# Performance work log

Hardware: AMD Instinct MI355X
Metric: run time of the kernel (lower is better)

Reference implementation:

```python
import jax, jax.numpy as jnp
import numpy as np

EPS_BN = 1e-5
K_INTERP = 8
K_NEIGH = 16


def _bn(x, g, b):
    # BatchNorm1d in training mode: batch stats over rows (biased var), eps=1e-5
    m = x.mean(axis=0)
    v = x.var(axis=0)
    return (x - m) * jax.lax.rsqrt(v + EPS_BN) * g + b


def _dist(a, b):
    # a:(B,N,3), b:(B,M,3) -> Euclidean distance (B,N,M), computed via the
    # quadratic expansion (clamped at 0) instead of materializing (B,N,M,3)
    d2 = (jnp.sum(a * a, -1)[:, :, None] + jnp.sum(b * b, -1)[:, None, :]
          - 2.0 * jnp.einsum('bnc,bmc->bnm', a, b))
    return jnp.sqrt(jnp.maximum(d2, 0.0))


def _gather(feats, idx):
    # feats:(B,M,C), idx:(B,N,K) int -> (B,N,K,C)
    return jax.vmap(lambda f, i: f[i])(feats, idx)


def setup_inputs() -> dict:
    key = jax.random.key(0)
    B, N1, N2, DS, DD, DOUT = 4, 4096, 1024, 128, 64, 256
    ks = jax.random.split(key, 20)
    s = 0.02
    inp = {
        'p1': jax.random.uniform(ks[0], (B * N1, 3), jnp.float32),
        'x1': jax.random.normal(ks[1], (B * N1, DD), jnp.float32),
        'o1': (jnp.arange(B, dtype=jnp.int32) + 1) * N1,
        'p2': jax.random.uniform(ks[2], (B * N2, 3), jnp.float32),
        'x2': jax.random.normal(ks[3], (B * N2, DS), jnp.float32),
        'o2': (jnp.arange(B, dtype=jnp.int32) + 1) * N2,
        'batch_size': B,
        # dense_mlp: Linear(DD,DS) + BN
        'W_dense': jax.random.normal(ks[4], (DD, DS), jnp.float32) * s,
        'b_dense': jnp.zeros((DS,), jnp.float32),
        'g_dense': jnp.ones((DS,), jnp.float32),
        'bt_dense': jnp.zeros((DS,), jnp.float32),
        # CrossAttentionPointTransformerLayer (dim=DS, hidden_mult=1)
        'Wq': jax.random.normal(ks[5], (DS, DS), jnp.float32) * s,
        'Wk': jax.random.normal(ks[6], (DS, DS), jnp.float32) * s,
        'Wv': jax.random.normal(ks[7], (DS, DS), jnp.float32) * s,
        'W1': jax.random.normal(ks[8], (DS, DS), jnp.float32) * s,
        'b1': jnp.zeros((DS,), jnp.float32),
        'g1': jnp.ones((DS,), jnp.float32),
        'bt1': jnp.zeros((DS,), jnp.float32),
        'W2': jax.random.normal(ks[9], (DS, DS), jnp.float32) * s,
        'b2': jnp.zeros((DS,), jnp.float32),
        # output mlp: Linear(DS+DD, DOUT) + BN
        'W_out': jax.random.normal(ks[10], (DS + DD, DOUT), jnp.float32) * s,
        'b_out': jnp.zeros((DOUT,), jnp.float32),
        'g_out': jnp.ones((DOUT,), jnp.float32),
        'bt_out': jnp.zeros((DOUT,), jnp.float32),
    }
    return inp


def reference(p1, x1, o1, p2, x2, o2, batch_size,
              W_dense, b_dense, g_dense, bt_dense,
              Wq, Wk, Wv, W1, b1, g1, bt1, W2, b2,
              W_out, b_out, g_out, bt_out):
    B = int(batch_size)
    N1 = p1.shape[0] // B
    N2 = p2.shape[0] // B
    DS = x2.shape[-1]

    # dense_mlp
    x1_dense = jax.nn.relu(_bn(x1 @ W_dense + b_dense, g_dense, bt_dense))  # (B*N1, DS)

    # pointops.interpolation(p2, p1, x2, o2, o1, k=8): inverse-distance kNN interp
    p1b = p1.reshape(B, N1, 3)
    p2b = p2.reshape(B, N2, 3)
    x2b = x2.reshape(B, N2, DS)
    d12 = _dist(p1b, p2b)                       # (B,N1,N2)
    negd, idx = jax.lax.top_k(-d12, K_INTERP)   # k nearest in p2
    dknn = -negd
    recip = 1.0 / (dknn + 1e-8)
    w = recip / recip.sum(-1, keepdims=True)    # (B,N1,8)
    x2_interp = jnp.einsum('bnk,bnkc->bnc', w, _gather(x2b, idx))  # (B,N1,DS)

    # CrossAttentionPointTransformerLayer(x_e=x1_dense, x_r=x_d=x2_interp, pos=p1)
    x_e = x1_dense.reshape(B, N1, DS)
    q = x_e @ Wq
    k = x2_interp @ Wk
    v = x2_interp @ Wv
    rel_dist = _dist(p1b, p1b)                  # (B,N1,N1)
    _, nidx = jax.lax.top_k(-rel_dist, K_NEIGH) # 16 nearest neighbors
    kg = _gather(k, nidx)                        # (B,N1,16,DS)
    vg = _gather(v, nidx)
    xeg = _gather(x_e, nidx)
    qk_rel = q[:, :, None, :] - kg
    v2 = vg + xeg
    h = (qk_rel + xeg).reshape(-1, DS)           # (B*N1*16, DS)
    h = jax.nn.relu(_bn(h @ W1 + b1, g1, bt1))
    sim = (h @ W2 + b2).reshape(B, N1, K_NEIGH, DS)
    attn = jax.nn.softmax(sim, axis=-2)          # over neighbors
    agg = jnp.einsum('bnkc,bnkc->bnc', attn, v2).reshape(B * N1, DS)

    # output mlp
    x = jax.nn.relu(_bn(jnp.concatenate([agg, x1], axis=-1) @ W_out + b_out,
                        g_out, bt_out))
    return (p1, x, o1)
```

## Files before the change

kernel.cpp:

```cpp
#include <hip/hip_runtime.h>
#include <math.h>

#define BB 4
#define NN1 4096
#define NN2 1024
#define DS 128
#define DD 64
#define DOUT 256
#define M1 16384
#define MH 262144
#define KCAT 192
#define KI 8
#define KN 16

#define OUT_P1 49152
#define OUT_X  49152
#define OUT_O1 4243456


static const size_t OFF_HPRE = 0;
static const size_t OFF_WTS  = 16777216;
static const size_t OFF_TMP  = 33554432;
static const size_t OFF_XD   = OFF_TMP  + 2097152;
static const size_t OFF_XI   = OFF_XD   + 2097152;
static const size_t OFF_Q    = OFF_XI   + 2097152;
static const size_t OFF_K    = OFF_Q    + 2097152;
static const size_t OFF_V    = OFF_K    + 2097152;
static const size_t OFF_OUTP = OFF_V    + 2097152;
static const size_t OFF_NIDX = OFF_OUTP + 4194304;
static const size_t OFF_STAT = OFF_NIDX + 262144;
static const size_t OFF_P1Q  = OFF_STAT + 4096;
static const size_t OFF_P2Q  = OFF_P1Q  + 65536;
static const size_t OFF_P1S  = OFF_P2Q  + 16384;
static const size_t OFF_P2S  = OFF_P1S  + 65536;

#define WDH 0
#define WDL 8192
#define WQH 16384
#define WQL 32768
#define WKH 49152
#define WKL 65536
#define WVH 81920
#define WVL 98304
#define W1H 114688
#define W1L 131072
#define W2H 147456
#define W2L 163840
#define WOH 180224
#define WOL 229376

typedef __attribute__((ext_vector_type(8))) short short8;
typedef __attribute__((ext_vector_type(4))) float floatx4;
typedef __attribute__((ext_vector_type(2))) float float2v;

__device__ inline unsigned short f2bf(float f) {
    union { float f; unsigned int u; } x; x.f = f;
    unsigned int r = x.u + 0x7fffu + ((x.u >> 16) & 1u);
    return (unsigned short)(r >> 16);
}
__device__ inline float bf2f(unsigned short h) {
    union { unsigned int u; float f; } x; x.u = ((unsigned int)h) << 16;
    return x.f;
}
__device__ inline unsigned long long shfl_xor_u64(unsigned long long v, int m) {
    unsigned lo = (unsigned)v, hi = (unsigned)(v >> 32);
    lo = (unsigned)__shfl_xor((int)lo, m);
    hi = (unsigned)__shfl_xor((int)hi, m);
    return ((unsigned long long)hi << 32) | lo;
}
__device__ inline unsigned cvt_pk_bf16(float lo, float hi) {
    unsigned r;
    asm volatile("v_cvt_pk_bf16_f32 %0, %1, %2" : "=v"(r) : "v"(lo), "v"(hi));
    return r;
}

#define PRO_STAT  (OUT_P1 + BB)
#define PRO_PACK  (PRO_STAT + 3072)
#define PRO_TOTAL (PRO_PACK + M1 + BB*NN2)
#define NPRO 285
struct SwzParams {
    const float* W[7];
    unsigned short* hi[7];
    unsigned short* lo[7];
    int N[7];
    int fid0[8];
};
__global__ __launch_bounds__(256) void k_prolog(
    const float* __restrict__ p1, const int* __restrict__ o1,
    const float* __restrict__ p2, float* __restrict__ out,
    float* __restrict__ stat, float4* __restrict__ p1q,
    float4* __restrict__ p2q, float* __restrict__ p1s,
    float* __restrict__ p2s, SwzParams p)
{
    if (blockIdx.x < NPRO) {
        int i = blockIdx.x * 256 + threadIdx.x;
        if (i < OUT_P1) out[i] = p1[i];
        else if (i < PRO_STAT) out[OUT_O1 + (i - OUT_P1)] = (float)o1[i - OUT_P1];
        else if (i < PRO_PACK) stat[i - PRO_STAT] = 0.f;
        else if (i < PRO_TOTAL) {
            int j = i - PRO_PACK;
            const float* src; float4* dst; float* ps; int jj;
            if (j < M1) { src = p1; dst = p1q; ps = p1s; jj = j; }
            else        { src = p2; dst = p2q; ps = p2s; jj = j - M1; }
            float x = src[jj*3+0] * 16384.f;
            float y = src[jj*3+1] * 16384.f;
            float z = src[jj*3+2] * 16384.f;
            float n = fmaf(z, z, fmaf(y, y, x*x));
            dst[jj] = make_float4(x, y, z, n);
            int pb8 = (jj >> 1)*8 + (jj & 1);
            ps[pb8]   = x + x; ps[pb8+2] = y + y;
            ps[pb8+4] = z + z; ps[pb8+6] = n;
        }
        return;
    }
    int fid = (blockIdx.x - NPRO)*4 + (threadIdx.x >> 6);
    int lane = threadIdx.x & 63;
    if (fid >= 272) return;
    int seg = 0;
    #pragma unroll
    for (int i = 1; i < 7; i++) if (fid >= p.fid0[i]) seg = i;
    int f = fid - p.fid0[seg];
    const float* W = p.W[seg];
    int N = p.N[seg];
    int ncj = N >> 4;
    int slab = f / ncj, cj = f - slab*ncj;
    int n  = cj*16 + (lane & 15);
    int k0 = slab*32 + (lane >> 4)*8;
    unsigned int oh[8], ol[8];
    #pragma unroll
    for (int j = 0; j < 8; j++) {
        float v = W[(size_t)(k0 + j) * N + n];
        unsigned short h = f2bf(v);
        oh[j] = h;
        ol[j] = f2bf(v - bf2f(h));
    }
    uint4 ph, pl;
    ph.x = oh[0] | (oh[1] << 16); ph.y = oh[2] | (oh[3] << 16);
    ph.z = oh[4] | (oh[5] << 16); ph.w = oh[6] | (oh[7] << 16);
    pl.x = ol[0] | (ol[1] << 16); pl.y = ol[2] | (ol[3] << 16);
    pl.z = ol[4] | (ol[5] << 16); pl.w = ol[6] | (ol[7] << 16);
    ((uint4*)p.hi[seg])[f*64 + lane] = ph;
    ((uint4*)p.lo[seg])[f*64 + lane] = pl;
}

template<int N, int K, int MODE, int STATS, int BNA>
__global__ __launch_bounds__(256) void k_gemm_mf(
    const float* __restrict__ Amat, const unsigned short* __restrict__ Whi,
    const unsigned short* __restrict__ Wlo, const float* __restrict__ bias,
    float* __restrict__ C, const float* __restrict__ aux,
    float* __restrict__ sums, float* __restrict__ sumsq,
    const float* __restrict__ bsums, const float* __restrict__ bsumsq,
    const float* __restrict__ bg, const float* __restrict__ bbt)
{
    __shared__ float sstat[STATS ? 2*N : 1];
    __shared__ float sbn[BNA ? 2*DS : 1];
    const int t = threadIdx.x, w = t >> 6, lane = t & 63;
    const int quad = lane >> 4, c = lane & 15;
    const int row = blockIdx.x*64 + w*16 + c;
    const int sA = (MODE == 2) ? DS : K;
    constexpr int nslab = K >> 5;
    constexpr int ncj = N >> 4;
    const int seg = (MODE == 3) ? blockIdx.y : 0;
    const float* Abase = (MODE == 3 && seg > 0) ? aux : Amat;
    const unsigned short* WhiS = Whi + (size_t)seg*32768;
    const unsigned short* WloS = Wlo + (size_t)seg*32768;
    float* CS = C + (size_t)seg*2097152;
    unsigned short* CS16 = (unsigned short*)C + (size_t)seg*4194304;
    if (STATS) {
        for (int i = t; i < 2*N; i += 256) sstat[i] = 0.f;
    }
    if (BNA) {
        if (t < DS) {
            const float invM = 1.f / (float)M1;
            float m   = bsums[t] * invM;
            float var = bsumsq[t] * invM - m*m;
            float sc  = bg[t] * rsqrtf(var + 1e-5f);
            sbn[t] = sc;
            sbn[DS + t] = bbt[t] - m * sc;
        }
    }
    if (STATS || BNA) __syncthreads();

    floatx4 acc[ncj];
    #pragma unroll
    for (int cj = 0; cj < ncj; cj++) acc[cj] = (floatx4){0.f,0.f,0.f,0.f};

    #pragma unroll
    for (int slab = 0; slab < nslab; slab++) {
        const int kk = slab*32 + quad*8;
        const float* src;
        if (MODE == 2 && kk >= DS) src = aux + (size_t)row*DD + (kk - DS);
        else                       src = Abase + (size_t)row*sA + kk;
        floatx4 va = *(const floatx4*)src;
        floatx4 vb = *(const floatx4*)(src + 4);
        if (BNA && MODE == 3 && seg == 0) {
            #pragma unroll
            for (int j = 0; j < 4; j++) {
                va[j] = fmaxf(fmaf(va[j], sbn[kk+j],   sbn[DS+kk+j]),   0.f);
                vb[j] = fmaxf(fmaf(vb[j], sbn[kk+4+j], sbn[DS+kk+4+j]), 0.f);
            }
        }
        short8 ahi, alo;
        #pragma unroll
        for (int j = 0; j < 4; j++) {
            unsigned short h = f2bf(va[j]);
            ahi[j] = (short)h; alo[j] = (short)f2bf(va[j] - bf2f(h));
        }
        #pragma unroll
        for (int j = 0; j < 4; j++) {
            unsigned short h = f2bf(vb[j]);
            ahi[4+j] = (short)h; alo[4+j] = (short)f2bf(vb[j] - bf2f(h));
        }
        const short8* bh = (const short8*)WhiS + (size_t)slab*ncj*64;
        const short8* bl = (const short8*)WloS + (size_t)slab*ncj*64;
        #pragma unroll
        for (int cj = 0; cj < ncj; cj++) {
            short8 bhv = bh[cj*64 + lane];
            short8 blv = bl[cj*64 + lane];
            acc[cj] = __builtin_amdgcn_mfma_f32_16x16x32_bf16(alo, bhv, acc[cj], 0, 0, 0);
            acc[cj] = __builtin_amdgcn_mfma_f32_16x16x32_bf16(ahi, blv, acc[cj], 0, 0, 0);
            acc[cj] = __builtin_amdgcn_mfma_f32_16x16x32_bf16(ahi, bhv, acc[cj], 0, 0, 0);
        }
    }
    const int rbase = blockIdx.x*64 + w*16 + quad*4;
    #pragma unroll
    for (int cj = 0; cj < ncj; cj++) {
        const float bb = bias ? bias[cj*16 + c] : 0.f;
        float s = 0.f, ss = 0.f;
        #pragma unroll
        for (int p = 0; p < 4; p++) {
            float v = acc[cj][p] + bb;
            if (MODE == 3) {
                if (seg > 0) {
                    float xv = Amat[(size_t)(rbase + p)*DS + cj*16 + c];
                    if (BNA) xv = fmaxf(fmaf(xv, sbn[cj*16+c], sbn[DS+cj*16+c]), 0.f);
                    if (seg == 1) v = xv - v;
                    else          v += xv;
                }
                CS16[(size_t)(rbase + p)*N + cj*16 + c] = f2bf(v);
            } else {
                CS[(size_t)(rbase + p)*N + cj*16 + c] = v;
            }
            if (STATS) { s += v; ss += v*v; }
        }
        if (STATS) {
            s  += __shfl_xor(s, 16);  s  += __shfl_xor(s, 32);
            ss += __shfl_xor(ss, 16); ss += __shfl_xor(ss, 32);
            if (quad == 0) {
                atomicAdd(&sstat[cj*16 + c], s);
                atomicAdd(&sstat[N + cj*16 + c], ss);
            }
        }
    }
    if (STATS) {
        __syncthreads();
        for (int i = t; i < N; i += 256) {
            atomicAdd(&sums[i],  sstat[i]);
            atomicAdd(&sumsq[i], sstat[N + i]);
        }
    }
}

__global__ __launch_bounds__(256) void k_gemm_qe(
    const unsigned short* __restrict__ q16, const unsigned short* __restrict__ e16,
    const unsigned short* __restrict__ W1hi, const float* __restrict__ b1,
    float* __restrict__ qw, float* __restrict__ ew)
{
    const int t = threadIdx.x, w = t >> 6, lane = t & 63;
    const int quad = lane >> 4, c = lane & 15;
    const int y = blockIdx.y;
    const unsigned short* A = y ? e16 : q16;
    float* C = y ? ew : qw;
    const int row = blockIdx.x*64 + w*16 + c;

    floatx4 acc[8];
    #pragma unroll
    for (int cj = 0; cj < 8; cj++) acc[cj] = (floatx4){0.f,0.f,0.f,0.f};

    #pragma unroll
    for (int slab = 0; slab < 4; slab++) {
        uint4 av = *(const uint4*)(A + (size_t)row*DS + slab*32 + quad*8);
        short8 af;
        ((uint4*)&af)[0] = av;
        const short8* bh = (const short8*)W1hi + (size_t)slab*8*64;
        #pragma unroll
        for (int cj = 0; cj < 8; cj++) {
            short8 bhv = bh[cj*64 + lane];
            acc[cj] = __builtin_amdgcn_mfma_f32_16x16x32_bf16(af, bhv, acc[cj], 0, 0, 0);
        }
    }
    const int rbase = blockIdx.x*64 + w*16 + quad*4;
    #pragma unroll
    for (int cj = 0; cj < 8; cj++) {
        const float bb = y ? b1[cj*16 + c] : 0.f;
        #pragma unroll
        for (int p = 0; p < 4; p++)
            C[(size_t)(rbase + p)*DS + cj*16 + c] = acc[cj][p] + bb;
    }
}

__global__ __launch_bounds__(256) void k_hstat(
    const float* __restrict__ qw, const float* __restrict__ ew,
    const int* __restrict__ nidx,
    float* __restrict__ sums, float* __restrict__ sumsq)
{
    __shared__ float sstat[256];
    const int t = threadIdx.x, w = t >> 6, lane = t & 63;
    sstat[t] = 0.f;
    __syncthreads();
    const int col = lane*2;
    float Sx = 0.f, Sy = 0.f, SSx = 0.f, SSy = 0.f;
    #pragma unroll
    for (int g2 = 0; g2 < 4; g2++) {
        const int gp = blockIdx.x*16 + w*4 + g2;
        float2 a = *(const float2*)(qw + (size_t)gp*DS + col);
        float B1x = 0.f, B1y = 0.f, B2x = 0.f, B2y = 0.f;
        const int* np = nidx + gp*16;
        #pragma unroll
        for (int cc = 0; cc < 16; cc++) {
            int m = np[cc];
            float2 b = *(const float2*)(ew + (size_t)m*DS + col);
            B1x += b.x; B1y += b.y;
            B2x = fmaf(b.x, b.x, B2x); B2y = fmaf(b.y, b.y, B2y);
        }
        Sx += fmaf(16.f, a.x, B1x);
        Sy += fmaf(16.f, a.y, B1y);
        SSx += fmaf(16.f*a.x, a.x, fmaf(2.f*a.x, B1x, B2x));
        SSy += fmaf(16.f*a.y, a.y, fmaf(2.f*a.y, B1y, B2y));
    }
    atomicAdd(&sstat[col],       Sx); atomicAdd(&sstat[col+1],       Sy);
    atomicAdd(&sstat[128 + col], SSx); atomicAdd(&sstat[128 + col+1], SSy);
    __syncthreads();
    if (t < 128) atomicAdd(&sums[t], sstat[t]);
    else         atomicAdd(&sumsq[t - 128], sstat[t]);
}

__global__ __launch_bounds__(256) void k_attn3(
    const float* __restrict__ qw, const float* __restrict__ ew,
    const float* __restrict__ sums_h, const float* __restrict__ sumsq_h,
    const float* __restrict__ g1, const float* __restrict__ bt1,
    const unsigned short* __restrict__ W2sw,
    const unsigned short* __restrict__ v, const int* __restrict__ nidx,
    float* __restrict__ agg)
{
    __shared__ unsigned short WF[16384];
    __shared__ float s_sc[DS], s_sh[DS];
    const int t = threadIdx.x;
    #pragma unroll
    for (int i = 0; i < 8; i++)
        ((uint4*)WF)[t + 256*i] = ((const uint4*)W2sw)[t + 256*i];
    if (t < DS) {
        const float invM = 1.f / (float)MH;
        float m   = sums_h[t] * invM;
        float var = sumsq_h[t] * invM - m*m;
        float sc  = g1[t] * rsqrtf(var + 1e-5f);
        s_sc[t] = sc;
        s_sh[t] = bt1[t] - m * sc;
    }
    __syncthreads();

    const int w = t >> 6, lane = t & 63;
    const int gp = blockIdx.x * 4 + w;
    const int quad = lane >> 4, c = lane & 15;
    const int mrow = nidx[gp*16 + c];

    floatx4 acc[8];
    #pragma unroll
    for (int cj = 0; cj < 8; cj++) acc[cj] = (floatx4){0.f, 0.f, 0.f, 0.f};

    for (int ks = 0; ks < 4; ks++) {
        const int ko = ks*32 + quad*8;
        const float* qp = qw + (size_t)gp*DS + ko;
        const float* ep = ew + (size_t)mrow*DS + ko;
        floatx4 qa = *(const floatx4*)qp;
        floatx4 qb = *(const floatx4*)(qp + 4);
        floatx4 ea = *(const floatx4*)ep;
        floatx4 eb = *(const floatx4*)(ep + 4);
        floatx4 sc0 = *(const floatx4*)&s_sc[ko];
        floatx4 sc1 = *(const floatx4*)&s_sc[ko + 4];
        floatx4 sh0 = *(const floatx4*)&s_sh[ko];
        floatx4 sh1 = *(const floatx4*)&s_sh[ko + 4];
        float f[8];
        #pragma unroll
        for (int j = 0; j < 4; j++) {
            f[j]   = fmaxf(fmaf(qa[j] + ea[j], sc0[j], sh0[j]), 0.f);
            f[4+j] = fmaxf(fmaf(qb[j] + eb[j], sc1[j], sh1[j]), 0.f);
        }
        short8 af;
        #pragma unroll
        for (int j = 0; j < 4; j++)
            ((unsigned*)&af)[j] = cvt_pk_bf16(f[2*j], f[2*j+1]);
        #pragma unroll
        for (int cj = 0; cj < 8; cj++) {
            short8 bfv = ((const short8*)WF)[(ks*8 + cj)*64 + lane];
            acc[cj] = __builtin_amdgcn_mfma_f32_16x16x32_bf16(af, bfv, acc[cj], 0, 0, 0);
        }
    }

    int nid[4];
    #pragma unroll
    for (int p = 0; p < 4; p++) nid[p] = nidx[gp*16 + quad*4 + p];

    #pragma unroll
    for (int cj = 0; cj < 8; cj++) {
        float m4 = fmaxf(fmaxf(acc[cj][0], acc[cj][1]), fmaxf(acc[cj][2], acc[cj][3]));
        m4 = fmaxf(m4, __shfl_xor(m4, 16));
        m4 = fmaxf(m4, __shfl_xor(m4, 32));
        float e[4]; float s4 = 0.f;
        #pragma unroll
        for (int p = 0; p < 4; p++) { e[p] = __expf(acc[cj][p] - m4); s4 += e[p]; }
        s4 += __shfl_xor(s4, 16); s4 += __shfl_xor(s4, 32);
        const float inv = 1.f / s4;
        const int col = cj*16 + c;
        float a = 0.f;
        #pragma unroll
        for (int p = 0; p < 4; p++)
            a = fmaf(e[p]*inv, bf2f(v[(size_t)nid[p]*DS + col]), a);
        a += __shfl_xor(a, 16); a += __shfl_xor(a, 32);
        if (quad == 0) agg[(size_t)gp*DS + col] = a;
    }
}

__global__ __launch_bounds__(256) void k_bnrelu(
    const float4* __restrict__ X, const float* __restrict__ sums,
    const float* __restrict__ sumsq, const float* __restrict__ g,
    const float* __restrict__ bt, float invM,
    float4* __restrict__ Y, size_t total4, int N)
{
    size_t i = (size_t)blockIdx.x * 256 + threadIdx.x;
    if (i < total4) {
        int c = (int)((i*4) & (size_t)(N - 1));
        float4 sm = *(const float4*)(sums + c);
        float4 sq = *(const float4*)(sumsq + c);
        float4 gg = *(const float4*)(g + c);
        float4 bb = *(const float4*)(bt + c);
        float4 x = X[i], y;
        float m0 = sm.x*invM, m1 = sm.y*invM, m2 = sm.z*invM, m3 = sm.w*invM;
        float s0 = gg.x*rsqrtf(sq.x*invM - m0*m0 + 1e-5f);
        float s1 = gg.y*rsqrtf(sq.y*invM - m1*m1 + 1e-5f);
        float s2 = gg.z*rsqrtf(sq.z*invM - m2*m2 + 1e-5f);
        float s3 = gg.w*rsqrtf(sq.w*invM - m3*m3 + 1e-5f);
        y.x = fmaxf(fmaf(x.x, s0, bb.x - m0*s0), 0.f);
        y.y = fmaxf(fmaf(x.y, s1, bb.y - m1*s1), 0.f);
        y.z = fmaxf(fmaf(x.z, s2, bb.z - m2*s2), 0.f);
        y.w = fmaxf(fmaf(x.w, s3, bb.w - m3*s3), 0.f);
        Y[i] = y;
    }
}

template<int NCAND, int KSEL, int EPI, int CAP>
__device__ __forceinline__ void sel_body(
    int gp0,
    const float4* __restrict__ qpts4, const float4* __restrict__ cpts4,
    const float* __restrict__ cpairs,
    int* __restrict__ nidx, const float* __restrict__ x2, float* __restrict__ xi,
    unsigned* hist0, unsigned* hist1,
    unsigned* skey, unsigned* sidx,
    float* swtE, unsigned* sidxE,
    unsigned* wpart, int* sstate)
{
    const int b = gp0 >> 12;
    const int t = threadIdx.x, wv = t >> 6, lane = t & 63;
    constexpr int ITER  = NCAND / 256;
    constexpr int PITER = NCAND / 512;

    const float4 qv0 = qpts4[gp0];
    const float4 qv1 = qpts4[gp0 + 1];
    const float4* pb = cpts4 + (size_t)b*NCAND;
    const float*  pbs = cpairs + (size_t)b*NCAND*4;

    unsigned kreg[2][ITER];
    if (t < 16)      ((uint4*)hist0)[t]      = (uint4){0u,0u,0u,0u};
    else if (t < 32) ((uint4*)hist1)[t - 16] = (uint4){0u,0u,0u,0u};
    __syncthreads();

    {
        const float2v nqx0 = {-qv0.x, -qv0.x}, nqy0 = {-qv0.y, -qv0.y};
        const float2v nqz0 = {-qv0.z, -qv0.z}, qw0 = {qv0.w, qv0.w};
        const float2v nqx1 = {-qv1.x, -qv1.x}, nqy1 = {-qv1.y, -qv1.y};
        const float2v nqz1 = {-qv1.z, -qv1.z}, qw1 = {qv1.w, qv1.w};
        #pragma unroll
        for (int pi = 0; pi < PITER; pi++) {
            const int ip = t + 256*pi;
            float4 A  = ((const float4*)pbs)[2*ip];
            float4 Bv = ((const float4*)pbs)[2*ip + 1];
            float2v xp = {A.x, A.y},  yp = {A.z, A.w};
            float2v zp = {Bv.x, Bv.y}, wp = {Bv.z, Bv.w};
            float2v d0 = wp + qw0;
            d0 = __builtin_elementwise_fma(xp, nqx0, d0);
            d0 = __builtin_elementwise_fma(yp, nqy0, d0);
            d0 = __builtin_elementwise_fma(zp, nqz0, d0);
            float2v d1 = wp + qw1;
            d1 = __builtin_elementwise_fma(xp, nqx1, d1);
            d1 = __builtin_elementwise_fma(yp, nqy1, d1);
            d1 = __builtin_elementwise_fma(zp, nqz1, d1);
            unsigned ka = (unsigned)d0[0], kb = (unsigned)d0[1];
            unsigned kc = (unsigned)d1[0], kd = (unsigned)d1[1];
            kreg[0][2*pi] = ka; kreg[0][2*pi+1] = kb;
            kreg[1][2*pi] = kc; kreg[1][2*pi+1] = kd;
            if ((ka >> 20) < CAP) atomicAdd(&hist0[ka >> 20], 1u);
            if ((kb >> 20) < CAP) atomicAdd(&hist0[kb >> 20], 1u);
            if ((kc >> 20) < CAP) atomicAdd(&hist1[kc >> 20], 1u);
            if ((kd >> 20) < CAP) atomicAdd(&hist1[kd >> 20], 1u);
        }
    }
    __syncthreads();

    if (wv < 2) {
        unsigned* H = wv ? hist1 : hist0;
        unsigned h = (lane < CAP) ? H[lane] : 0u;
        unsigned incl = h;
        #pragma unroll
        for (int off = 1; off < 64; off <<= 1) {
            unsigned o = (unsigned)__shfl_up((int)incl, off);
            if (lane >= off) incl += o;
        }
        unsigned excl = incl - h;
        const int base = wv*8;
        if ((int)excl < KSEL && KSEL <= (int)(excl + h)) {
            sstate[base+0] = lane; sstate[base+1] = (int)excl; sstate[base+2] = (int)h;
            sstate[base+3] = ((int)(excl + h) <= 64) ? 1 : 0;
            sstate[base+4] = 0;
        }
        unsigned tot = (unsigned)__shfl((int)incl, 63);
        if (lane == 0 && (int)tot < KSEL) sstate[base+3] = -1;
    }
    __syncthreads();

    if (sstate[3] == -1 || sstate[11] == -1) {
        for (int qi = 0; qi < 2; qi++) {
            if (sstate[qi*8+3] != -1) continue;
            ((uint4*)hist0)[t] = (uint4){0u,0u,0u,0u};
            __syncthreads();
            #pragma unroll
            for (int it = 0; it < ITER; it++)
                atomicAdd(&hist0[kreg[qi][it] >> 20], 1u);
            __syncthreads();
            uint4 h4 = ((const uint4*)hist0)[t];
            unsigned hv[4] = {h4.x, h4.y, h4.z, h4.w};
            unsigned tsum = hv[0]+hv[1]+hv[2]+hv[3];
            unsigned incl = tsum;
            #pragma unroll
            for (int off = 1; off < 64; off <<= 1) {
                unsigned o = (unsigned)__shfl_up((int)incl, off);
                if (lane >= off) incl += o;
            }
            if (lane == 63) wpart[wv] = incl;
            __syncthreads();
            unsigned wbase = 0;
            for (int i2 = 0; i2 < wv; i2++) wbase += wpart[i2];
            unsigned excl = wbase + incl - tsum;
            if ((int)excl < KSEL && KSEL <= (int)(excl + tsum)) {
                unsigned cum = excl;
                #pragma unroll
                for (int i2 = 0; i2 < 4; i2++) {
                    unsigned h = hv[i2];
                    if ((int)cum < KSEL && KSEL <= (int)(cum + h)) {
                        sstate[qi*8+0] = t*4 + i2; sstate[qi*8+1] = (int)cum;
                        sstate[qi*8+2] = (int)h;
                        sstate[qi*8+3] = ((int)cum + (int)h <= 64) ? 1 : 0;
                        sstate[qi*8+4] = 0;
                        break;
                    }
                    cum += h;
                }
            }
            __syncthreads();
        }
    }

    if (sstate[3] == 1 && sstate[11] == 1) {
        const unsigned P0 = (unsigned)sstate[0];
        const unsigned P1 = (unsigned)sstate[8];
        #pragma unroll
        for (int pi = 0; pi < PITER; pi++) {
            const int ip = t + 256*pi;
            #pragma unroll
            for (int c2 = 0; c2 < 2; c2++) {
                const int j = 2*ip + c2;
                const unsigned k0 = kreg[0][2*pi+c2], k1 = kreg[1][2*pi+c2];
                if ((k0 >> 20) <= P0) {
                    int pos = (int)atomicAdd((unsigned*)&sstate[4], 1u);
                    skey[pos] = k0; sidx[pos] = (unsigned)j;
                }
                if ((k1 >> 20) <= P1) {
                    int pos = (int)atomicAdd((unsigned*)&sstate[12], 1u);
                    skey[64 + pos] = k1; sidx[64 + pos] = (unsigned)j;
                }
            }
        }
    } else {
        #pragma unroll
        for (int qi = 0; qi < 2; qi++) {
            const float4 qv = qi ? qv1 : qv0;
            unsigned P = (unsigned)sstate[qi*8+0];
            int S = sstate[qi*8+1], cntB = sstate[qi*8+2], mode = sstate[qi*8+3];
            int gsh = 20;
            if (mode == 0) {
                for (int round = 1; round < 4; round++) {
                    const int nb  = (round == 3) ? 16 : 256;
                    const int wb  = (round == 3) ? 4 : 8;
                    const int sh  = (round == 1) ? 12 : (round == 2 ? 4 : 0);
                    const int psh = sh + wb;
                    if (t < nb) hist0[t] = 0u;
                    __syncthreads();
                    #pragma unroll
                    for (int it = 0; it < ITER; it++) {
                        unsigned key = kreg[qi][it];
                        if ((key >> psh) == P)
                            atomicAdd(&hist0[(key >> sh) & (nb - 1)], 1u);
                    }
                    __syncthreads();
                    unsigned hv = (t < nb) ? hist0[t] : 0u;
                    unsigned tsum = hv;
                    unsigned incl = tsum;
                    #pragma unroll
                    for (int off = 1; off < 64; off <<= 1) {
                        unsigned o = (unsigned)__shfl_up((int)incl, off);
                        if (lane >= off) incl += o;
                    }
                    if (lane == 63) wpart[wv] = incl;
                    __syncthreads();
                    unsigned wbase = 0;
                    for (int i2 = 0; i2 < wv; i2++) wbase += wpart[i2];
                    unsigned exclT = wbase + incl - tsum;
                    const int need = KSEL - S;
                    if ((int)exclT < need && need <= (int)(exclT + tsum)) {
                        int Snew = S + (int)exclT;
                        int tot  = Snew + (int)tsum;
                        sstate[qi*8+0] = (int)((P << wb) | (unsigned)t);
                        sstate[qi*8+1] = Snew; sstate[qi*8+2] = (int)tsum;
                        sstate[qi*8+3] = (tot <= 64) ? 1 : ((round == 3) ? 2 : 0);
                        sstate[qi*8+4] = 0;
                    }
                    __syncthreads();
                    P = (unsigned)sstate[qi*8+0]; S = sstate[qi*8+1];
                    cntB = sstate[qi*8+2]; mode = sstate[qi*8+3];
                    gsh = sh;
                    if (mode) break;
                }
            }
            if (mode == 1) {
                #pragma unroll
                for (int pi = 0; pi < PITER; pi++) {
                    const int ip = t + 256*pi;
                    #pragma unroll
                    for (int c2 = 0; c2 < 2; c2++) {
                        const int j = 2*ip + c2;
                        unsigned key = kreg[qi][2*pi+c2];
                        if ((key >> gsh) <= P) {
                            int pos = (int)atomicAdd((unsigned*)&sstate[qi*8+4], 1u);
                            skey[qi*64 + pos] = key; sidx[qi*64 + pos] = (unsigned)j;
                        }
                    }
                }
            } else if (mode != 1) {
                if (t < 64) {
                    const unsigned long long lmask = (1ull << lane) - 1ull;
                    int cnt = 0;
                    for (int pass = 0; pass < 2; pass++) {
                        for (int it = 0; it < NCAND/64; it++) {
                            int j = lane + 64*it;
                            float4 cv = pb[j];
                            float dot = fmaf(qv.z, cv.z, fmaf(qv.y, cv.y, qv.x*cv.x));
                            float d2 = fmaxf(fmaf(-2.f, dot, qv.w + cv.w), 0.f);
                            unsigned key = (unsigned)d2;
                            bool f = pass ? (key == P) : (key < P);
                            unsigned long long bal = __ballot(f);
                            if (f) {
                                int pos = cnt + __popcll(bal & lmask);
                                if (pos < 64) { skey[qi*64 + pos] = key; sidx[qi*64 + pos] = (unsigned)j; }
                            }
                            cnt += __popcll(bal);
                        }
                    }
                    if (lane == 0) { sstate[qi*8+1] = min(cnt, 64); sstate[qi*8+2] = 0; }
                }
            }
            __syncthreads();
        }
    }
    __syncthreads();

    if (wv < 2) {
        const int q = wv;
        const int total = sstate[q*8+1] + sstate[q*8+2];
        unsigned long long v = ~0ull;
        if (lane < total)
            v = (((unsigned long long)skey[q*64 + lane]) << 32) | sidx[q*64 + lane];
        #pragma unroll
        for (int k = 2; k <= 64; k <<= 1) {
            #pragma unroll
            for (int jj = k >> 1; jj > 0; jj >>= 1) {
                unsigned long long p = shfl_xor_u64(v, jj);
                bool up = ((lane & k) == 0);
                bool takeMin = (((lane & jj) == 0) == up);
                bool pl = p < v;
                v = (takeMin == pl) ? p : v;
            }
        }
        if (EPI == 0) {
            if (lane < KSEL)
                nidx[(gp0 + q)*KSEL + lane] = b*NCAND + (int)(v & 0xffffffffull);
        } else {
            const float4 qq = q ? qv1 : qv0;
            float wgt = 0.f;
            unsigned si = (unsigned)(v & 0xffffffffull);
            if (lane < KSEL) {
                float4 cv = pb[si];
                float dot = fmaf(qq.z, cv.z, fmaf(qq.y, cv.y, qq.x*cv.x));
                float d2 = fmaxf(fmaf(-2.f, dot, qq.w + cv.w), 0.f);
                wgt = 1.f / (sqrtf(d2) + 1.6384e-4f);
            }
            float ws = wgt;
            ws += __shfl_xor(ws, 1); ws += __shfl_xor(ws, 2); ws += __shfl_xor(ws, 4);
            if (lane < KSEL) {
                swtE[q*KSEL + lane]  = wgt / ws;
                sidxE[q*KSEL + lane] = si;
            }
        }
    }

    if (EPI == 1) {
        __syncthreads();
        const int qi2 = t >> 7, tt = t & 127;
        const float* x2b = x2 + (size_t)b*NCAND*DS;
        float a = 0.f;
        #pragma unroll
        for (int r = 0; r < KSEL; r++)
            a = fmaf(swtE[qi2*KSEL + r], x2b[(size_t)sidxE[qi2*KSEL + r]*DS + tt], a);
        xi[(size_t)(gp0 + qi2)*DS + tt] = a;
    }
}

__global__ __launch_bounds__(256) void k_sel2(
    const float4* __restrict__ p1q, const float4* __restrict__ p2q,
    const float* __restrict__ p1s, const float* __restrict__ p2s,
    int* __restrict__ nidx, const float* __restrict__ x2, float* __restrict__ xi)
{
    __shared__ __align__(16) unsigned hist0[1024], hist1[1024];
    __shared__ __align__(16) unsigned skey[128], sidx[128];
    __shared__ float    swtE[2*KI];
    __shared__ unsigned sidxE[2*KI];
    __shared__ unsigned wpart[8];
    __shared__ int      sstate[20];
    const int bid = blockIdx.x;
    if (bid < M1/2) {
        sel_body<NN1, KN, 0, 32>(bid*2, p1q, p1q, p1s, nidx, nullptr, nullptr,
                                 hist0, hist1, skey, sidx, swtE, sidxE, wpart, sstate);
    } else {
        sel_body<NN2, KI, 1, 64>((bid - M1/2)*2, p1q, p2q, p2s, nullptr, x2, xi,
                                 hist0, hist1, skey, sidx, swtE, sidxE, wpart, sstate);
    }
}

extern "C" void kernel_launch(void* const* d_in, const int* in_sizes, int n_in,
                              void* d_out, int out_size, void* d_ws, size_t ws_size,
                              hipStream_t stream)
{
    const float* p1 = (const float*)d_in[0];
    const float* x1 = (const float*)d_in[1];
    const int*   o1 = (const int*)d_in[2];
    const float* p2 = (const float*)d_in[3];
    const float* x2 = (const float*)d_in[4];
    const float* W_dense = (const float*)d_in[7];
    const float* b_dense = (const float*)d_in[8];
    const float* g_dense = (const float*)d_in[9];
    const float* bt_dense= (const float*)d_in[10];
    const float* Wq = (const float*)d_in[11];
    const float* Wk = (const float*)d_in[12];
    const float* Wv = (const float*)d_in[13];
    const float* W1 = (const float*)d_in[14];
    const float* b1 = (const float*)d_in[15];
    const float* g1 = (const float*)d_in[16];
    const float* bt1= (const float*)d_in[17];
    const float* W2 = (const float*)d_in[18];
    const float* W_out = (const float*)d_in[20];
    const float* b_out = (const float*)d_in[21];
    const float* g_out = (const float*)d_in[22];
    const float* bt_out= (const float*)d_in[23];

    float* ws   = (float*)d_ws;
    unsigned short* wts  = (unsigned short*)(ws + OFF_WTS);
    float* tmp  = ws + OFF_TMP;
    float* qw1f = ws + OFF_XD;
    float* ew1f = ws + OFF_OUTP;
    float* xi   = ws + OFF_XI;
    float* qm   = ws + OFF_Q;
    float* outp = ws + OFF_OUTP;
    int*   nidx = (int*)(ws + OFF_NIDX);
    float* stat = ws + OFF_STAT;
    float4* p1q = (float4*)(ws + OFF_P1Q);
    float4* p2q = (float4*)(ws + OFF_P2Q);
    float* p1s = ws + OFF_P1S;
    float* p2s = ws + OFF_P2S;
    unsigned short* q16 = (unsigned short*)(ws + OFF_Q);
    unsigned short* e16 = (unsigned short*)(ws + OFF_K);
    unsigned short* v16 = (unsigned short*)(ws + OFF_V);
    float* sums_d = stat,      *sumsq_d = stat+256;
    float* sums_h = stat+1024, *sumsq_h = stat+1280;
    float* sums_o = stat+2048, *sumsq_o = stat+2304;
    float* out = (float*)d_out;

    SwzParams sp;
    sp.W[0]=W_dense; sp.W[1]=Wq; sp.W[2]=Wk; sp.W[3]=Wv; sp.W[4]=W1; sp.W[5]=W2; sp.W[6]=W_out;
    sp.hi[0]=wts+WDH; sp.hi[1]=wts+WQH; sp.hi[2]=wts+WKH; sp.hi[3]=wts+WVH;
    sp.hi[4]=wts+W1H; sp.hi[5]=wts+W2H; sp.hi[6]=wts+WOH;
    sp.lo[0]=wts+WDL; sp.lo[1]=wts+WQL; sp.lo[2]=wts+WKL; sp.lo[3]=wts+WVL;
    sp.lo[4]=wts+W1L; sp.lo[5]=wts+W2L; sp.lo[6]=wts+WOL;
    sp.N[0]=128; sp.N[1]=128; sp.N[2]=128; sp.N[3]=128; sp.N[4]=128; sp.N[5]=128; sp.N[6]=256;
    sp.fid0[0]=0; sp.fid0[1]=16; sp.fid0[2]=48; sp.fid0[3]=80; sp.fid0[4]=112;
    sp.fid0[5]=144; sp.fid0[6]=176; sp.fid0[7]=272;
    k_prolog<<<NPRO + 68, 256, 0, stream>>>(p1, o1, p2, out, stat, p1q, p2q, p1s, p2s, sp);

    k_sel2<<<M1, 256, 0, stream>>>(p1q, p2q, p1s, p2s, nidx, x2, xi);

    k_gemm_mf<128,64,0,1,0><<<M1/64, 256, 0, stream>>>(x1, wts+WDH, wts+WDL, b_dense, tmp,
        nullptr, sums_d, sumsq_d, nullptr, nullptr, nullptr, nullptr);

    k_gemm_mf<128,128,3,0,1><<<dim3(M1/64,3), 256, 0, stream>>>(tmp, wts+WQH, wts+WQL,
        nullptr, qm, xi, nullptr, nullptr, sums_d, sumsq_d, g_dense, bt_dense);

    k_gemm_qe<<<dim3(M1/64, 2), 256, 0, stream>>>(q16, e16, wts+W1H, b1, qw1f, ew1f);
    k_hstat<<<M1/16, 256, 0, stream>>>(qw1f, ew1f, nidx, sums_h, sumsq_h);

    k_attn3<<<M1/4, 256, 0, stream>>>(qw1f, ew1f, sums_h, sumsq_h, g1, bt1,
        wts+W2H, v16, nidx, tmp);

    k_gemm_mf<256,192,2,1,0><<<M1/64, 256, 0, stream>>>(tmp, wts+WOH, wts+WOL, b_out, outp,
        x1, sums_o, sumsq_o, nullptr, nullptr, nullptr, nullptr);
    k_bnrelu<<<(M1*DOUT/4)/256, 256, 0, stream>>>((const float4*)outp, sums_o, sumsq_o,
        g_out, bt_out, 1.f/(float)M1, (float4*)(out + OUT_X), (size_t)M1*DOUT/4, DOUT);
}
```

Measured before the change: 322.0 us.

## Fold W1 into Wq/Wk products and store attention projections as bf16

Precomputes Wq·W1 and -Wk·W1 in the prolog so the Q-side and E-side W1 projections come directly out of the projection GEMMs. The separate k_gemm_qe pass and its fp32 intermediate buffers go away. The E-side becomes one K=256 GEMM over concatenated [x_e, x_interp] inputs, with BN+ReLU applied only to the x_e half. hstat and attn3 now read bf16 projections instead of fp32, which halves gather traffic at the cost of rounding error.

```diff
diff --git a/kernel.cpp b/kernel.cpp
--- a/kernel.cpp
+++ b/kernel.cpp
@@ -18,7 +18,6 @@
 #define OUT_O1 4243456
 
 
-static const size_t OFF_HPRE = 0;
 static const size_t OFF_WTS  = 16777216;
 static const size_t OFF_TMP  = 33554432;
 static const size_t OFF_XD   = OFF_TMP  + 2097152;
@@ -36,18 +35,16 @@
 
 #define WDH 0
 #define WDL 8192
-#define WQH 16384
-#define WQL 32768
-#define WKH 49152
-#define WKL 65536
+#define WQW1H 16384
+#define WQW1L 32768
 #define WVH 81920
 #define WVL 98304
-#define W1H 114688
-#define W1L 131072
-#define W2H 147456
-#define W2L 163840
-#define WOH 180224
-#define WOL 229376
+#define WEH 114688
+#define WEL 147456
+#define W2H 180224
+#define W2L 196608
+#define WOH 212992
+#define WOL 262144
 
 typedef __attribute__((ext_vector_type(8))) short short8;
 typedef __attribute__((ext_vector_type(4))) float floatx4;
@@ -79,11 +76,14 @@
 #define PRO_TOTAL (PRO_PACK + M1 + BB*NN2)
 #define NPRO 285
 struct SwzParams {
-    const float* W[7];
-    unsigned short* hi[7];
-    unsigned short* lo[7];
-    int N[7];
-    int fid0[8];
+    const float* W[5];
+    unsigned short* hi[5];
+    unsigned short* lo[5];
+    const float* Wq; const float* Wk; const float* W1r;
+    unsigned short* phi[2];
+    unsigned short* plo[2];
+    int N[5];
+    int fid0[5];
 };
 __global__ __launch_bounds__(256) void k_prolog(
     const float* __restrict__ p1, const int* __restrict__ o1,
@@ -116,31 +116,57 @@
     int fid = (blockIdx.x - NPRO)*4 + (threadIdx.x >> 6);
     int lane = threadIdx.x & 63;
     if (fid >= 272) return;
-    int seg = 0;
-    #pragma unroll
-    for (int i = 1; i < 7; i++) if (fid >= p.fid0[i]) seg = i;
-    int f = fid - p.fid0[seg];
-    const float* W = p.W[seg];
-    int N = p.N[seg];
-    int ncj = N >> 4;
-    int slab = f / ncj, cj = f - slab*ncj;
-    int n  = cj*16 + (lane & 15);
-    int k0 = slab*32 + (lane >> 4)*8;
+    float vsrc[8];
+    unsigned short* hiD; unsigned short* loD; int fstore;
+    if (fid < 208) {
+        int seg = 0;
+        #pragma unroll
+        for (int i = 1; i < 5; i++) if (fid >= p.fid0[i]) seg = i;
+        int f = fid - p.fid0[seg];
+        const float* W = p.W[seg];
+        int N = p.N[seg];
+        int ncj = N >> 4;
+        int slab = f / ncj, cj = f - slab*ncj;
+        int n  = cj*16 + (lane & 15);
+        int k0 = slab*32 + (lane >> 4)*8;
+        #pragma unroll
+        for (int j = 0; j < 8; j++) vsrc[j] = W[(size_t)(k0 + j) * N + n];
+        hiD = p.hi[seg]; loD = p.lo[seg]; fstore = f;
+    } else {
+        int pf = fid - 208;
+        int which = pf >> 5;
+        int f = pf & 31;
+        const float* Wa = which ? p.Wk : p.Wq;
+        int slab = f >> 3, cj = f & 7;
+        int n  = cj*16 + (lane & 15);
+        int k0 = slab*32 + (lane >> 4)*8;
+        float acc[8];
+        #pragma unroll
+        for (int j = 0; j < 8; j++) acc[j] = 0.f;
+        for (int m = 0; m < 128; m++) {
+            float wc = p.W1r[m*128 + n];
+            #pragma unroll
+            for (int j = 0; j < 8; j++)
+                acc[j] = fmaf(Wa[(size_t)(k0 + j)*128 + m], wc, acc[j]);
+        }
+        #pragma unroll
+        for (int j = 0; j < 8; j++) vsrc[j] = which ? -acc[j] : acc[j];
+        hiD = p.phi[which]; loD = p.plo[which]; fstore = f;
+    }
     unsigned int oh[8], ol[8];
     #pragma unroll
     for (int j = 0; j < 8; j++) {
-        float v = W[(size_t)(k0 + j) * N + n];
-        unsigned short h = f2bf(v);
+        unsigned short h = f2bf(vsrc[j]);
         oh[j] = h;
-        ol[j] = f2bf(v - bf2f(h));
+        ol[j] = f2bf(vsrc[j] - bf2f(h));
     }
     uint4 ph, pl;
     ph.x = oh[0] | (oh[1] << 16); ph.y = oh[2] | (oh[3] << 16);
     ph.z = oh[4] | (oh[5] << 16); ph.w = oh[6] | (oh[7] << 16);
     pl.x = ol[0] | (ol[1] << 16); pl.y = ol[2] | (ol[3] << 16);
     pl.z = ol[4] | (ol[5] << 16); pl.w = ol[6] | (ol[7] << 16);
-    ((uint4*)p.hi[seg])[f*64 + lane] = ph;
-    ((uint4*)p.lo[seg])[f*64 + lane] = pl;
+    ((uint4*)hiD)[fstore*64 + lane] = ph;
+    ((uint4*)loD)[fstore*64 + lane] = pl;
 }
 
 template<int N, int K, int MODE, int STATS, int BNA>
@@ -157,11 +183,11 @@
     const int t = threadIdx.x, w = t >> 6, lane = t & 63;
     const int quad = lane >> 4, c = lane & 15;
     const int row = blockIdx.x*64 + w*16 + c;
-    const int sA = (MODE == 2) ? DS : K;
+    const int sA = (MODE == 2 || MODE == 5) ? DS : K;
     constexpr int nslab = K >> 5;
     constexpr int ncj = N >> 4;
-    const int seg = (MODE == 3) ? blockIdx.y : 0;
-    const float* Abase = (MODE == 3 && seg > 0) ? aux : Amat;
+    const int seg = (MODE == 4) ? (int)blockIdx.y * 2 : 0;
+    const float* Abase = (MODE == 4 && seg > 0) ? aux : Amat;
     const unsigned short* WhiS = Whi + (size_t)seg*32768;
     const unsigned short* WloS = Wlo + (size_t)seg*32768;
     float* CS = C + (size_t)seg*2097152;
@@ -189,11 +215,12 @@
     for (int slab = 0; slab < nslab; slab++) {
         const int kk = slab*32 + quad*8;
         const float* src;
-        if (MODE == 2 && kk >= DS) src = aux + (size_t)row*DD + (kk - DS);
-        else                       src = Abase + (size_t)row*sA + kk;
+        if (MODE == 2 && kk >= DS)      src = aux + (size_t)row*DD + (kk - DS);
+        else if (MODE == 5 && kk >= DS) src = aux + (size_t)row*DS + (kk - DS);
+        else                            src = Abase + (size_t)row*sA + kk;
         floatx4 va = *(const floatx4*)src;
         floatx4 vb = *(const floatx4*)(src + 4);
-        if (BNA && MODE == 3 && seg == 0) {
+        if (BNA && ((MODE == 4 && seg == 0) || (MODE == 5 && kk < DS))) {
             #pragma unroll
             for (int j = 0; j < 4; j++) {
                 va[j] = fmaxf(fmaf(va[j], sbn[kk+j],   sbn[DS+kk+j]),   0.f);
@@ -230,12 +257,11 @@
         #pragma unroll
         for (int p = 0; p < 4; p++) {
             float v = acc[cj][p] + bb;
-            if (MODE == 3) {
-                if (seg > 0) {
+            if (MODE >= 4) {
+                if (MODE == 4 && seg > 0) {
                     float xv = Amat[(size_t)(rbase + p)*DS + cj*16 + c];
                     if (BNA) xv = fmaxf(fmaf(xv, sbn[cj*16+c], sbn[DS+cj*16+c]), 0.f);
-                    if (seg == 1) v = xv - v;
-                    else          v += xv;
+                    v += xv;
                 }
                 CS16[(size_t)(rbase + p)*N + cj*16 + c] = f2bf(v);
             } else {
@@ -261,46 +287,8 @@
     }
 }
 
-__global__ __launch_bounds__(256) void k_gemm_qe(
-    const unsigned short* __restrict__ q16, const unsigned short* __restrict__ e16,
-    const unsigned short* __restrict__ W1hi, const float* __restrict__ b1,
-    float* __restrict__ qw, float* __restrict__ ew)
-{
-    const int t = threadIdx.x, w = t >> 6, lane = t & 63;
-    const int quad = lane >> 4, c = lane & 15;
-    const int y = blockIdx.y;
-    const unsigned short* A = y ? e16 : q16;
-    float* C = y ? ew : qw;
-    const int row = blockIdx.x*64 + w*16 + c;
-
-    floatx4 acc[8];
-    #pragma unroll
-    for (int cj = 0; cj < 8; cj++) acc[cj] = (floatx4){0.f,0.f,0.f,0.f};
-
-    #pragma unroll
-    for (int slab = 0; slab < 4; slab++) {
-        uint4 av = *(const uint4*)(A + (size_t)row*DS + slab*32 + quad*8);
-        short8 af;
-        ((uint4*)&af)[0] = av;
-        const short8* bh = (const short8*)W1hi + (size_t)slab*8*64;
-        #pragma unroll
-        for (int cj = 0; cj < 8; cj++) {
-            short8 bhv = bh[cj*64 + lane];
-            acc[cj] = __builtin_amdgcn_mfma_f32_16x16x32_bf16(af, bhv, acc[cj], 0, 0, 0);
-        }
-    }
-    const int rbase = blockIdx.x*64 + w*16 + quad*4;
-    #pragma unroll
-    for (int cj = 0; cj < 8; cj++) {
-        const float bb = y ? b1[cj*16 + c] : 0.f;
-        #pragma unroll
-        for (int p = 0; p < 4; p++)
-            C[(size_t)(rbase + p)*DS + cj*16 + c] = acc[cj][p] + bb;
-    }
-}
-
 __global__ __launch_bounds__(256) void k_hstat(
-    const float* __restrict__ qw, const float* __restrict__ ew,
+    const unsigned short* __restrict__ qw, const unsigned short* __restrict__ ew,
     const int* __restrict__ nidx,
     float* __restrict__ sums, float* __restrict__ sumsq)
 {
@@ -313,20 +301,24 @@
     #pragma unroll
     for (int g2 = 0; g2 < 4; g2++) {
         const int gp = blockIdx.x*16 + w*4 + g2;
-        float2 a = *(const float2*)(qw + (size_t)gp*DS + col);
+        unsigned av = *(const unsigned*)(qw + (size_t)gp*DS + col);
+        float ax = bf2f((unsigned short)(av & 0xffffu));
+        float ay = bf2f((unsigned short)(av >> 16));
         float B1x = 0.f, B1y = 0.f, B2x = 0.f, B2y = 0.f;
         const int* np = nidx + gp*16;
         #pragma unroll
         for (int cc = 0; cc < 16; cc++) {
             int m = np[cc];
-            float2 b = *(const float2*)(ew + (size_t)m*DS + col);
-            B1x += b.x; B1y += b.y;
-            B2x = fmaf(b.x, b.x, B2x); B2y = fmaf(b.y, b.y, B2y);
-        }
-        Sx += fmaf(16.f, a.x, B1x);
-        Sy += fmaf(16.f, a.y, B1y);
-        SSx += fmaf(16.f*a.x, a.x, fmaf(2.f*a.x, B1x, B2x));
-        SSy += fmaf(16.f*a.y, a.y, fmaf(2.f*a.y, B1y, B2y));
+            unsigned bv = *(const unsigned*)(ew + (size_t)m*DS + col);
+            float bx = bf2f((unsigned short)(bv & 0xffffu));
+            float by = bf2f((unsigned short)(bv >> 16));
+            B1x += bx; B1y += by;
+            B2x = fmaf(bx, bx, B2x); B2y = fmaf(by, by, B2y);
+        }
+        Sx += fmaf(16.f, ax, B1x);
+        Sy += fmaf(16.f, ay, B1y);
+        SSx += fmaf(16.f*ax, ax, fmaf(2.f*ax, B1x, B2x));
+        SSy += fmaf(16.f*ay, ay, fmaf(2.f*ay, B1y, B2y));
     }
     atomicAdd(&sstat[col],       Sx); atomicAdd(&sstat[col+1],       Sy);
     atomicAdd(&sstat[128 + col], SSx); atomicAdd(&sstat[128 + col+1], SSy);
@@ -336,7 +328,7 @@
 }
 
 __global__ __launch_bounds__(256) void k_attn3(
-    const float* __restrict__ qw, const float* __restrict__ ew,
+    const unsigned short* __restrict__ qw, const unsigned short* __restrict__ ew,
     const float* __restrict__ sums_h, const float* __restrict__ sumsq_h,
     const float* __restrict__ g1, const float* __restrict__ bt1,
     const unsigned short* __restrict__ W2sw,
@@ -370,26 +362,25 @@
 
     for (int ks = 0; ks < 4; ks++) {
         const int ko = ks*32 + quad*8;
-        const float* qp = qw + (size_t)gp*DS + ko;
-        const float* ep = ew + (size_t)mrow*DS + ko;
-        floatx4 qa = *(const floatx4*)qp;
-        floatx4 qb = *(const floatx4*)(qp + 4);
-        floatx4 ea = *(const floatx4*)ep;
-        floatx4 eb = *(const floatx4*)(ep + 4);
+        uint4 qv4 = *(const uint4*)(qw + (size_t)gp*DS + ko);
+        uint4 ev4 = *(const uint4*)(ew + (size_t)mrow*DS + ko);
         floatx4 sc0 = *(const floatx4*)&s_sc[ko];
         floatx4 sc1 = *(const floatx4*)&s_sc[ko + 4];
         floatx4 sh0 = *(const floatx4*)&s_sh[ko];
         floatx4 sh1 = *(const floatx4*)&s_sh[ko + 4];
-        float f[8];
+        unsigned qwv[4] = {qv4.x, qv4.y, qv4.z, qv4.w};
+        unsigned ewv[4] = {ev4.x, ev4.y, ev4.z, ev4.w};
+        short8 af;
         #pragma unroll
         for (int j = 0; j < 4; j++) {
-            f[j]   = fmaxf(fmaf(qa[j] + ea[j], sc0[j], sh0[j]), 0.f);
-            f[4+j] = fmaxf(fmaf(qb[j] + eb[j], sc1[j], sh1[j]), 0.f);
-        }
-        short8 af;
-        #pragma unroll
-        for (int j = 0; j < 4; j++)
-            ((unsigned*)&af)[j] = cvt_pk_bf16(f[2*j], f[2*j+1]);
+            float h0 = bf2f((unsigned short)(qwv[j] & 0xffffu))
+                     + bf2f((unsigned short)(ewv[j] & 0xffffu));
+            float h1 = bf2f((unsigned short)(qwv[j] >> 16))
+                     + bf2f((unsigned short)(ewv[j] >> 16));
+            float f0 = fmaxf(fmaf(h0, (j<2)?sc0[2*j]:sc1[2*j-4],   (j<2)?sh0[2*j]:sh1[2*j-4]),   0.f);
+            float f1 = fmaxf(fmaf(h1, (j<2)?sc0[2*j+1]:sc1[2*j-3], (j<2)?sh0[2*j+1]:sh1[2*j-3]), 0.f);
+            ((unsigned*)&af)[j] = cvt_pk_bf16(f0, f1);
+        }
         #pragma unroll
         for (int cj = 0; cj < 8; cj++) {
             short8 bfv = ((const short8*)WF)[(ks*8 + cj)*64 + lane];
@@ -783,8 +774,6 @@
     float* ws   = (float*)d_ws;
     unsigned short* wts  = (unsigned short*)(ws + OFF_WTS);
     float* tmp  = ws + OFF_TMP;
-    float* qw1f = ws + OFF_XD;
-    float* ew1f = ws + OFF_OUTP;
     float* xi   = ws + OFF_XI;
     float* qm   = ws + OFF_Q;
     float* outp = ws + OFF_OUTP;
@@ -794,23 +783,23 @@
     float4* p2q = (float4*)(ws + OFF_P2Q);
     float* p1s = ws + OFF_P1S;
     float* p2s = ws + OFF_P2S;
-    unsigned short* q16 = (unsigned short*)(ws + OFF_Q);
-    unsigned short* e16 = (unsigned short*)(ws + OFF_K);
-    unsigned short* v16 = (unsigned short*)(ws + OFF_V);
+    unsigned short* qw16 = (unsigned short*)(ws + OFF_Q);
+    unsigned short* ew16 = (unsigned short*)(ws + OFF_K);
+    unsigned short* v16  = (unsigned short*)(ws + OFF_V);
     float* sums_d = stat,      *sumsq_d = stat+256;
     float* sums_h = stat+1024, *sumsq_h = stat+1280;
     float* sums_o = stat+2048, *sumsq_o = stat+2304;
     float* out = (float*)d_out;
 
     SwzParams sp;
-    sp.W[0]=W_dense; sp.W[1]=Wq; sp.W[2]=Wk; sp.W[3]=Wv; sp.W[4]=W1; sp.W[5]=W2; sp.W[6]=W_out;
-    sp.hi[0]=wts+WDH; sp.hi[1]=wts+WQH; sp.hi[2]=wts+WKH; sp.hi[3]=wts+WVH;
-    sp.hi[4]=wts+W1H; sp.hi[5]=wts+W2H; sp.hi[6]=wts+WOH;
-    sp.lo[0]=wts+WDL; sp.lo[1]=wts+WQL; sp.lo[2]=wts+WKL; sp.lo[3]=wts+WVL;
-    sp.lo[4]=wts+W1L; sp.lo[5]=wts+W2L; sp.lo[6]=wts+WOL;
-    sp.N[0]=128; sp.N[1]=128; sp.N[2]=128; sp.N[3]=128; sp.N[4]=128; sp.N[5]=128; sp.N[6]=256;
+    sp.W[0]=W_dense; sp.W[1]=Wv; sp.W[2]=W1; sp.W[3]=W2; sp.W[4]=W_out;
+    sp.hi[0]=wts+WDH; sp.hi[1]=wts+WVH; sp.hi[2]=wts+WEH; sp.hi[3]=wts+W2H; sp.hi[4]=wts+WOH;
+    sp.lo[0]=wts+WDL; sp.lo[1]=wts+WVL; sp.lo[2]=wts+WEL; sp.lo[3]=wts+W2L; sp.lo[4]=wts+WOL;
+    sp.Wq=Wq; sp.Wk=Wk; sp.W1r=W1;
+    sp.phi[0]=wts+WQW1H; sp.phi[1]=wts+WEH+16384;
+    sp.plo[0]=wts+WQW1L; sp.plo[1]=wts+WEL+16384;
+    sp.N[0]=128; sp.N[1]=128; sp.N[2]=128; sp.N[3]=128; sp.N[4]=256;
     sp.fid0[0]=0; sp.fid0[1]=16; sp.fid0[2]=48; sp.fid0[3]=80; sp.fid0[4]=112;
-    sp.fid0[5]=144; sp.fid0[6]=176; sp.fid0[7]=272;
     k_prolog<<<NPRO + 68, 256, 0, stream>>>(p1, o1, p2, out, stat, p1q, p2q, p1s, p2s, sp);
 
     k_sel2<<<M1, 256, 0, stream>>>(p1q, p2q, p1s, p2s, nidx, x2, xi);
@@ -818,13 +807,15 @@
     k_gemm_mf<128,64,0,1,0><<<M1/64, 256, 0, stream>>>(x1, wts+WDH, wts+WDL, b_dense, tmp,
         nullptr, sums_d, sumsq_d, nullptr, nullptr, nullptr, nullptr);
 
-    k_gemm_mf<128,128,3,0,1><<<dim3(M1/64,3), 256, 0, stream>>>(tmp, wts+WQH, wts+WQL,
+    k_gemm_mf<128,128,4,0,1><<<dim3(M1/64,2), 256, 0, stream>>>(tmp, wts+WQW1H, wts+WQW1L,
         nullptr, qm, xi, nullptr, nullptr, sums_d, sumsq_d, g_dense, bt_dense);
 
-    k_gemm_qe<<<dim3(M1/64, 2), 256, 0, stream>>>(q16, e16, wts+W1H, b1, qw1f, ew1f);
-    k_hstat<<<M1/16, 256, 0, stream>>>(qw1f, ew1f, nidx, sums_h, sumsq_h);
-
-    k_attn3<<<M1/4, 256, 0, stream>>>(qw1f, ew1f, sums_h, sumsq_h, g1, bt1,
+    k_gemm_mf<128,256,5,0,1><<<M1/64, 256, 0, stream>>>(tmp, wts+WEH, wts+WEL,
+        b1, ws + OFF_K, xi, nullptr, nullptr, sums_d, sumsq_d, g_dense, bt_dense);
+
+    k_hstat<<<M1/16, 256, 0, stream>>>(qw16, ew16, nidx, sums_h, sumsq_h);
+
+    k_attn3<<<M1/4, 256, 0, stream>>>(qw16, ew16, sums_h, sumsq_h, g1, bt1,
         wts+W2H, v16, nidx, tmp);
 
     k_gemm_mf<256,192,2,1,0><<<M1/64, 256, 0, stream>>>(tmp, wts+WOH, wts+WOL, b_out, outp,
```

After: 336.1 us. +4.4%, slower.
